# Kernel optimization log

Measured on AMD Instinct MI355X. Metric: run time of the kernel, lower is better.

Reference implementation:

```python
import jax, jax.numpy as jnp
import numpy as np

EPS = 1e-12  # matches torch F.normalize eps


def _l2_normalize(x, axis):
    n = jnp.linalg.norm(x, axis=axis, keepdims=True)
    return x / jnp.maximum(n, EPS)


def setup_inputs() -> dict:
    key = jax.random.key(0)
    k1, k2 = jax.random.split(key)
    B, C, h, w = 16, 64, 21, 21
    n_classes, M = 10, 2205  # M = shot(5) * h*w(441)
    x1 = jax.random.normal(k1, (B, C, h, w), dtype=jnp.float32)
    x2 = jax.random.normal(k2, (n_classes, C, M), dtype=jnp.float32)
    return {"x1": x1, "x2": x2, "neighbor_k": 3}


def reference(x1, x2, neighbor_k):
    B, C, h, w = x1.shape
    # queries: [B, h*w, C] local descriptors, L2-normalized per descriptor
    q = _l2_normalize(x1.reshape(B, C, h * w).transpose(0, 2, 1), axis=-1)
    # support: [n, C, M], normalized along channel dim (torch dim=0 per class)
    s = _l2_normalize(x2, axis=1)
    # all pairwise cosine similarities: [B, n, h*w, M]
    inner = jnp.einsum('bqc,ncm->bnqm', q, s)
    topv, _ = jax.lax.top_k(inner, neighbor_k)  # [B, n, h*w, k]
    return topv.sum(axis=(2, 3))  # [B, n]
```

## Files before the change

kernel.cpp:

```cpp
#include <hip/hip_runtime.h>
#include <math.h>

#define BB    16
#define CC    64
#define HW    441
#define QP    448
#define NCLS  10
#define MM    2205
#define MP2   2304
#define CH_T  8
#define CH_B  (CH_T * 16 * CC * 2)
#define NCH   18
#define NQT   4
#define NQG   7

typedef _Float16 half8 __attribute__((ext_vector_type(8)));
typedef float   float4_ __attribute__((ext_vector_type(4)));

#define WAIT_VMCNT(n) __builtin_amdgcn_s_waitcnt(0x0F70 | (n))

#define GLDS16(g, l) __builtin_amdgcn_global_load_lds(                         \
    (const __attribute__((address_space(1))) unsigned int*)(const void*)(g),   \
    (__attribute__((address_space(3))) unsigned int*)(void*)(l), 16, 0, 0)

__device__ __forceinline__ void ins3(float d, float& a0, float& a1, float& a2) {
    float n0 = fmaxf(d, a0);
    float n1 = __builtin_amdgcn_fmed3f(d, a0, a1);
    float n2 = __builtin_amdgcn_fmed3f(d, a1, a2);
    a0 = n0; a1 = n1; a2 = n2;
}

__global__ __launch_bounds__(256) void prep(const float* __restrict__ x1,
                                            const float* __restrict__ x2,
                                            _Float16* __restrict__ qn,
                                            _Float16* __restrict__ sn) {
    __shared__ float ssred[256];
    __shared__ half8 obuf[256];
    int tid = threadIdx.x;
    int ml = tid & 31, cg = tid >> 5;
    float v[8];
    half8* dstblk;
    int wz;
    if (blockIdx.x < BB * 14) {
        int b = blockIdx.x / 14, pt = blockIdx.x % 14;
        int p = pt * 32 + ml;
        const float* src = x1 + (size_t)b * CC * HW + p;
        bool real = p < HW;
        #pragma unroll
        for (int i = 0; i < 8; ++i) v[i] = real ? src[(size_t)(cg * 8 + i) * HW] : 0.f;
        wz = cg;
        dstblk = (half8*)(qn + ((size_t)(b * QP + pt * 32)) * CC);
    } else {
        int sb = blockIdx.x - BB * 14;
        int n = sb / 72, mt = sb % 72;
        int m = mt * 32 + ml;
        const float* src = x2 + (size_t)n * CC * MM + m;
        bool real = m < MM;
        #pragma unroll
        for (int i = 0; i < 8; ++i) v[i] = real ? src[(size_t)(cg * 8 + i) * MM] : 0.f;
        wz = cg ^ (ml & 7);
        dstblk = (half8*)(sn + ((size_t)(n * MP2 + mt * 32)) * CC);
    }
    float ss = 0.f;
    #pragma unroll
    for (int i = 0; i < 8; ++i) ss += v[i] * v[i];
    ssred[tid] = ss;
    __syncthreads();
    float tot = 0.f;
    #pragma unroll
    for (int j = 0; j < 8; ++j) tot += ssred[j * 32 + ml];
    float inv = 1.f / fmaxf(sqrtf(tot), 1e-12f);
    half8 h;
    #pragma unroll
    for (int i = 0; i < 8; ++i) h[i] = (_Float16)(v[i] * inv);
    obuf[ml * 8 + wz] = h;
    __syncthreads();
    dstblk[tid] = obuf[tid];
}

__global__ __launch_bounds__(256, 4) void img2class_mfma(const _Float16* __restrict__ qn,
                                                         const _Float16* __restrict__ sn,
                                                         float* __restrict__ out) {
    __shared__ half8 ldsv[2 * CH_T * 16 * 8];
    _Float16* ldsh = (_Float16*)ldsv;
    char* lbase = (char*)ldsv;

    int t  = blockIdx.x;
    int bn = t / NQG, qg = t % NQG;
    int b = bn / NCLS, n = bn % NCLS;

    int tid  = threadIdx.x;
    int wave = tid >> 6, lane = tid & 63;
    int col  = lane & 15, quad = lane >> 4;
    int q0 = qg * (NQT * 16);

    const char* sbase = (const char*)(sn + (size_t)n * MP2 * CC);
    int so   = wave * 4096 + lane * 16;
    int ldst = wave * 4096;

    #pragma unroll
    for (int i = 0; i < 4; ++i)
        GLDS16(sbase + so + i * 1024, lbase + ldst + i * 1024);

    const half8* Qp = (const half8*)(qn + ((size_t)(b * QP + q0 + col)) * CC) + quad;
    half8 Q0[NQT], Q1[NQT];
    #pragma unroll
    for (int qt = 0; qt < NQT; ++qt) {
        Q0[qt] = Qp[qt * 128];
        Q1[qt] = Qp[qt * 128 + 4];
    }

    float T0[NQT], T1[NQT], T2[NQT];
    #pragma unroll
    for (int qt = 0; qt < NQT; ++qt) { T0[qt] = -1.0e30f; T1[qt] = -1.0e30f; T2[qt] = -1.0e30f; }

    int offE0 = col * CC + ((quad       ^ (col & 7)) << 3);
    int offE1 = col * CC + (((4 + quad) ^ (col & 7)) << 3);

    for (int c = 0; c < NCH; ++c) {
        if (c + 1 < NCH) {
            __builtin_amdgcn_sched_barrier(0);
            const char* g = sbase + (size_t)(c + 1) * CH_B + so;
            char* l = lbase + ((c + 1) & 1) * CH_B + ldst;
            #pragma unroll
            for (int i = 0; i < 4; ++i)
                GLDS16(g + i * 1024, l + i * 1024);
            WAIT_VMCNT(4);
        } else {
            WAIT_VMCNT(0);
        }
        __builtin_amdgcn_sched_barrier(0);

        const _Float16* lw = ldsh + (c & 1) * (CH_T * 16 * CC) + wave * (32 * CC);
        half8 S0e = *(const half8*)(lw + offE0);
        half8 S1e = *(const half8*)(lw + offE1);
        half8 S0o = *(const half8*)(lw + offE0 + 16 * CC);
        half8 S1o = *(const half8*)(lw + offE1 + 16 * CC);

        int tE = c * CH_T + wave * 2;
        bool dopen = (tE >= 136);
        float pE0 = 0.f, pE1 = 0.f, pE2 = 0.f, pE3 = 0.f;
        float pO0 = 0.f, pO1 = 0.f, pO2 = 0.f, pO3 = 0.f;
        if (dopen) {
            int mE = tE * 16 + quad * 4;
            pE0 = (mE +  0 >= MM) ? -1.0e30f : 0.f;
            pE1 = (mE +  1 >= MM) ? -1.0e30f : 0.f;
            pE2 = (mE +  2 >= MM) ? -1.0e30f : 0.f;
            pE3 = (mE +  3 >= MM) ? -1.0e30f : 0.f;
            pO0 = (mE + 16 >= MM) ? -1.0e30f : 0.f;
            pO1 = (mE + 17 >= MM) ? -1.0e30f : 0.f;
            pO2 = (mE + 18 >= MM) ? -1.0e30f : 0.f;
            pO3 = (mE + 19 >= MM) ? -1.0e30f : 0.f;
        }

        float4_ z = {0.f, 0.f, 0.f, 0.f};
        #pragma unroll
        for (int qt = 0; qt < NQT; ++qt) {
            float4_ ae = __builtin_amdgcn_mfma_f32_16x16x32_f16(S0e, Q0[qt], z, 0, 0, 0);
            ae = __builtin_amdgcn_mfma_f32_16x16x32_f16(S1e, Q1[qt], ae, 0, 0, 0);
            float4_ ao = __builtin_amdgcn_mfma_f32_16x16x32_f16(S0o, Q0[qt], z, 0, 0, 0);
            ao = __builtin_amdgcn_mfma_f32_16x16x32_f16(S1o, Q1[qt], ao, 0, 0, 0);
            if (dopen) {
                ae.x += pE0; ae.y += pE1; ae.z += pE2; ae.w += pE3;
                ao.x += pO0; ao.y += pO1; ao.z += pO2; ao.w += pO3;
            }
            float d0 = fmaxf(ae.x, ao.x);
            float d1 = fmaxf(ae.y, ao.y);
            float d2 = fmaxf(ae.z, ao.z);
            float d3 = fmaxf(ae.w, ao.w);
            ins3(d0, T0[qt], T1[qt], T2[qt]);
            ins3(d1, T0[qt], T1[qt], T2[qt]);
            ins3(d2, T0[qt], T1[qt], T2[qt]);
            ins3(d3, T0[qt], T1[qt], T2[qt]);
        }
    }

    #pragma unroll
    for (int step = 16; step <= 32; step <<= 1) {
        #pragma unroll
        for (int qt = 0; qt < NQT; ++qt) {
            float o0 = __shfl_xor(T0[qt], step);
            float o1 = __shfl_xor(T1[qt], step);
            float o2 = __shfl_xor(T2[qt], step);
            ins3(o0, T0[qt], T1[qt], T2[qt]);
            ins3(o1, T0[qt], T1[qt], T2[qt]);
            ins3(o2, T0[qt], T1[qt], T2[qt]);
        }
    }

    float* dumpW = (float*)(lbase + wave * 4096);
    if (quad == 0) {
        #pragma unroll
        for (int qt = 0; qt < NQT; ++qt) {
            float* dp = dumpW + (qt * 16 + col) * 3;
            dp[0] = T0[qt]; dp[1] = T1[qt]; dp[2] = T2[qt];
        }
    }
    __syncthreads();

    float s = 0.f;
    if (tid < NQT * 16) {
        const float* d0 = (const float*)(lbase) + tid * 3;
        float a0 = d0[0], a1 = d0[1], a2 = d0[2];
        #pragma unroll
        for (int w = 1; w < 4; ++w) {
            const float* dw = (const float*)(lbase + w * 4096) + tid * 3;
            ins3(dw[0], a0, a1, a2);
            ins3(dw[1], a0, a1, a2);
            ins3(dw[2], a0, a1, a2);
        }
        s = a0 + a1 + a2;
    }
    #pragma unroll
    for (int step = 1; step < 64; step <<= 1) s += __shfl_xor(s, step);
    float* wsum = (float*)(lbase + CH_B);
    if (lane == 0) wsum[wave] = s;
    __syncthreads();
    if (tid == 0) atomicAdd(&out[bn], wsum[0] + wsum[1] + wsum[2] + wsum[3]);
}

extern "C" void kernel_launch(void* const* d_in, const int* in_sizes, int n_in,
                              void* d_out, int out_size, void* d_ws, size_t ws_size,
                              hipStream_t stream) {
    const float* x1 = (const float*)d_in[0];
    const float* x2 = (const float*)d_in[1];
    float* out = (float*)d_out;

    _Float16* qn = (_Float16*)d_ws;
    _Float16* sn = qn + (size_t)BB * QP * CC;

    hipMemsetAsync(d_out, 0, out_size, stream);
    prep<<<BB * 14 + NCLS * 72, 256, 0, stream>>>(x1, x2, qn, sn);
    img2class_mfma<<<BB * NCLS * NQG, 256, 0, stream>>>(qn, sn, out);
}
```

Before: 105.8 us.

## Share support chunks across all waves and split support dimension in halves

Every wave now processes all 128 support columns of each staged LDS chunk against its own 32 queries, so each block covers 128 queries instead of 64 and each chunk is reused across waves. The support dimension is split into two halves handled by separate blocks, with padding masked only on the final chunk. Per-query top-3 partials are written to workspace and combined by a new merge kernel, which replaces the atomics and the memset. The cost is extra block barriers per chunk, an extra kernel launch, and wasted work on padded queries (512 slots versus 441).

```diff
diff --git a/kernel.cpp b/kernel.cpp
--- a/kernel.cpp
+++ b/kernel.cpp
@@ -4,15 +4,14 @@
 #define BB    16
 #define CC    64
 #define HW    441
-#define QP    448
+#define QP2   512
 #define NCLS  10
 #define MM    2205
 #define MP2   2304
 #define CH_T  8
 #define CH_B  (CH_T * 16 * CC * 2)
-#define NCH   18
-#define NQT   4
-#define NQG   7
+#define NCH   9
+#define NQG   4
 
 typedef _Float16 half8 __attribute__((ext_vector_type(8)));
 typedef float   float4_ __attribute__((ext_vector_type(4)));
@@ -41,17 +40,17 @@
     float v[8];
     half8* dstblk;
     int wz;
-    if (blockIdx.x < BB * 14) {
-        int b = blockIdx.x / 14, pt = blockIdx.x % 14;
+    if (blockIdx.x < BB * 16) {
+        int b = blockIdx.x / 16, pt = blockIdx.x % 16;
         int p = pt * 32 + ml;
         const float* src = x1 + (size_t)b * CC * HW + p;
         bool real = p < HW;
         #pragma unroll
         for (int i = 0; i < 8; ++i) v[i] = real ? src[(size_t)(cg * 8 + i) * HW] : 0.f;
         wz = cg;
-        dstblk = (half8*)(qn + ((size_t)(b * QP + pt * 32)) * CC);
+        dstblk = (half8*)(qn + ((size_t)(b * QP2 + pt * 32)) * CC);
     } else {
-        int sb = blockIdx.x - BB * 14;
+        int sb = blockIdx.x - BB * 16;
         int n = sb / 72, mt = sb % 72;
         int m = mt * 32 + ml;
         const float* src = x2 + (size_t)n * CC * MM + m;
@@ -80,21 +79,23 @@
 
 __global__ __launch_bounds__(256, 4) void img2class_mfma(const _Float16* __restrict__ qn,
                                                          const _Float16* __restrict__ sn,
-                                                         float* __restrict__ out) {
+                                                         float* __restrict__ partial) {
     __shared__ half8 ldsv[2 * CH_T * 16 * 8];
     _Float16* ldsh = (_Float16*)ldsv;
     char* lbase = (char*)ldsv;
 
-    int t  = blockIdx.x;
+    int mh = blockIdx.x & 1;
+    int t  = blockIdx.x >> 1;
     int bn = t / NQG, qg = t % NQG;
     int b = bn / NCLS, n = bn % NCLS;
+    int mtile0 = mh ? 72 : 0;
 
     int tid  = threadIdx.x;
     int wave = tid >> 6, lane = tid & 63;
     int col  = lane & 15, quad = lane >> 4;
-    int q0 = qg * (NQT * 16);
-
-    const char* sbase = (const char*)(sn + (size_t)n * MP2 * CC);
+    int q0 = qg * 128;
+
+    const char* sbase = (const char*)(sn + (size_t)n * MP2 * CC) + (size_t)mtile0 * 16 * CC * 2;
     int so   = wave * 4096 + lane * 16;
     int ldst = wave * 4096;
 
@@ -102,24 +103,28 @@
     for (int i = 0; i < 4; ++i)
         GLDS16(sbase + so + i * 1024, lbase + ldst + i * 1024);
 
-    const half8* Qp = (const half8*)(qn + ((size_t)(b * QP + q0 + col)) * CC) + quad;
-    half8 Q0[NQT], Q1[NQT];
-    #pragma unroll
-    for (int qt = 0; qt < NQT; ++qt) {
-        Q0[qt] = Qp[qt * 128];
-        Q1[qt] = Qp[qt * 128 + 4];
-    }
-
-    float T0[NQT], T1[NQT], T2[NQT];
-    #pragma unroll
-    for (int qt = 0; qt < NQT; ++qt) { T0[qt] = -1.0e30f; T1[qt] = -1.0e30f; T2[qt] = -1.0e30f; }
-
-    int offE0 = col * CC + ((quad       ^ (col & 7)) << 3);
-    int offE1 = col * CC + (((4 + quad) ^ (col & 7)) << 3);
+    const half8* Qp = (const half8*)(qn + ((size_t)(b * QP2 + q0 + wave * 32 + col)) * CC) + quad;
+    half8 Q0[2], Q1[2];
+    #pragma unroll
+    for (int u = 0; u < 2; ++u) {
+        Q0[u] = Qp[u * 128];
+        Q1[u] = Qp[u * 128 + 4];
+    }
+
+    float T0[2], T1[2], T2[2];
+    #pragma unroll
+    for (int u = 0; u < 2; ++u) { T0[u] = -1.0e30f; T1[u] = -1.0e30f; T2[u] = -1.0e30f; }
+
+    int swz0 = (quad       ^ (col & 7)) << 3;
+    int swz1 = ((4 + quad) ^ (col & 7)) << 3;
+
+    float pO0 = (quad * 4 + 0 >= 13) ? -1.0e30f : 0.f;
+    float pO1 = (quad * 4 + 1 >= 13) ? -1.0e30f : 0.f;
+    float pO2 = (quad * 4 + 2 >= 13) ? -1.0e30f : 0.f;
+    float pO3 = (quad * 4 + 3 >= 13) ? -1.0e30f : 0.f;
 
     for (int c = 0; c < NCH; ++c) {
         if (c + 1 < NCH) {
-            __builtin_amdgcn_sched_barrier(0);
             const char* g = sbase + (size_t)(c + 1) * CH_B + so;
             char* l = lbase + ((c + 1) & 1) * CH_B + ldst;
             #pragma unroll
@@ -129,94 +134,84 @@
         } else {
             WAIT_VMCNT(0);
         }
+        __builtin_amdgcn_s_barrier();
         __builtin_amdgcn_sched_barrier(0);
 
-        const _Float16* lw = ldsh + (c & 1) * (CH_T * 16 * CC) + wave * (32 * CC);
-        half8 S0e = *(const half8*)(lw + offE0);
-        half8 S1e = *(const half8*)(lw + offE1);
-        half8 S0o = *(const half8*)(lw + offE0 + 16 * CC);
-        half8 S1o = *(const half8*)(lw + offE1 + 16 * CC);
-
-        int tE = c * CH_T + wave * 2;
-        bool dopen = (tE >= 136);
-        float pE0 = 0.f, pE1 = 0.f, pE2 = 0.f, pE3 = 0.f;
-        float pO0 = 0.f, pO1 = 0.f, pO2 = 0.f, pO3 = 0.f;
-        if (dopen) {
-            int mE = tE * 16 + quad * 4;
-            pE0 = (mE +  0 >= MM) ? -1.0e30f : 0.f;
-            pE1 = (mE +  1 >= MM) ? -1.0e30f : 0.f;
-            pE2 = (mE +  2 >= MM) ? -1.0e30f : 0.f;
-            pE3 = (mE +  3 >= MM) ? -1.0e30f : 0.f;
-            pO0 = (mE + 16 >= MM) ? -1.0e30f : 0.f;
-            pO1 = (mE + 17 >= MM) ? -1.0e30f : 0.f;
-            pO2 = (mE + 18 >= MM) ? -1.0e30f : 0.f;
-            pO3 = (mE + 19 >= MM) ? -1.0e30f : 0.f;
-        }
-
-        float4_ z = {0.f, 0.f, 0.f, 0.f};
-        #pragma unroll
-        for (int qt = 0; qt < NQT; ++qt) {
-            float4_ ae = __builtin_amdgcn_mfma_f32_16x16x32_f16(S0e, Q0[qt], z, 0, 0, 0);
-            ae = __builtin_amdgcn_mfma_f32_16x16x32_f16(S1e, Q1[qt], ae, 0, 0, 0);
-            float4_ ao = __builtin_amdgcn_mfma_f32_16x16x32_f16(S0o, Q0[qt], z, 0, 0, 0);
-            ao = __builtin_amdgcn_mfma_f32_16x16x32_f16(S1o, Q1[qt], ao, 0, 0, 0);
-            if (dopen) {
-                ae.x += pE0; ae.y += pE1; ae.z += pE2; ae.w += pE3;
-                ao.x += pO0; ao.y += pO1; ao.z += pO2; ao.w += pO3;
+        const _Float16* lw = ldsh + (c & 1) * (CH_T * 16 * CC);
+        bool lastc = (mh == 1) && (c == NCH - 1);
+        #pragma unroll
+        for (int p = 0; p < 4; ++p) {
+            if (lastc && p >= 1) break;
+            const _Float16* le = lw + (size_t)(p * 32 + col) * CC;
+            const _Float16* lo = le + 16 * CC;
+            half8 SA0 = *(const half8*)(le + swz0);
+            half8 SA1 = *(const half8*)(le + swz1);
+            half8 SB0 = *(const half8*)(lo + swz0);
+            half8 SB1 = *(const half8*)(lo + swz1);
+            float4_ z = {0.f, 0.f, 0.f, 0.f};
+            #pragma unroll
+            for (int u = 0; u < 2; ++u) {
+                float4_ ae = __builtin_amdgcn_mfma_f32_16x16x32_f16(SA0, Q0[u], z, 0, 0, 0);
+                ae = __builtin_amdgcn_mfma_f32_16x16x32_f16(SA1, Q1[u], ae, 0, 0, 0);
+                float4_ ao = __builtin_amdgcn_mfma_f32_16x16x32_f16(SB0, Q0[u], z, 0, 0, 0);
+                ao = __builtin_amdgcn_mfma_f32_16x16x32_f16(SB1, Q1[u], ao, 0, 0, 0);
+                if (lastc) { ao.x += pO0; ao.y += pO1; ao.z += pO2; ao.w += pO3; }
+                float d0 = fmaxf(ae.x, ao.x);
+                float d1 = fmaxf(ae.y, ao.y);
+                float d2 = fmaxf(ae.z, ao.z);
+                float d3 = fmaxf(ae.w, ao.w);
+                ins3(d0, T0[u], T1[u], T2[u]);
+                ins3(d1, T0[u], T1[u], T2[u]);
+                ins3(d2, T0[u], T1[u], T2[u]);
+                ins3(d3, T0[u], T1[u], T2[u]);
             }
-            float d0 = fmaxf(ae.x, ao.x);
-            float d1 = fmaxf(ae.y, ao.y);
-            float d2 = fmaxf(ae.z, ao.z);
-            float d3 = fmaxf(ae.w, ao.w);
-            ins3(d0, T0[qt], T1[qt], T2[qt]);
-            ins3(d1, T0[qt], T1[qt], T2[qt]);
-            ins3(d2, T0[qt], T1[qt], T2[qt]);
-            ins3(d3, T0[qt], T1[qt], T2[qt]);
-        }
+        }
+        __builtin_amdgcn_s_barrier();
     }
 
     #pragma unroll
     for (int step = 16; step <= 32; step <<= 1) {
         #pragma unroll
-        for (int qt = 0; qt < NQT; ++qt) {
-            float o0 = __shfl_xor(T0[qt], step);
-            float o1 = __shfl_xor(T1[qt], step);
-            float o2 = __shfl_xor(T2[qt], step);
-            ins3(o0, T0[qt], T1[qt], T2[qt]);
-            ins3(o1, T0[qt], T1[qt], T2[qt]);
-            ins3(o2, T0[qt], T1[qt], T2[qt]);
-        }
-    }
-
-    float* dumpW = (float*)(lbase + wave * 4096);
+        for (int u = 0; u < 2; ++u) {
+            float o0 = __shfl_xor(T0[u], step);
+            float o1 = __shfl_xor(T1[u], step);
+            float o2 = __shfl_xor(T2[u], step);
+            ins3(o0, T0[u], T1[u], T2[u]);
+            ins3(o1, T0[u], T1[u], T2[u]);
+            ins3(o2, T0[u], T1[u], T2[u]);
+        }
+    }
+
     if (quad == 0) {
         #pragma unroll
-        for (int qt = 0; qt < NQT; ++qt) {
-            float* dp = dumpW + (qt * 16 + col) * 3;
-            dp[0] = T0[qt]; dp[1] = T1[qt]; dp[2] = T2[qt];
-        }
-    }
+        for (int u = 0; u < 2; ++u) {
+            float* pp = partial + ((size_t)((bn * NQG + qg) * 2 + mh) * 128
+                                   + (wave * 2 + u) * 16 + col) * 3;
+            pp[0] = T0[u]; pp[1] = T1[u]; pp[2] = T2[u];
+        }
+    }
+}
+
+__global__ __launch_bounds__(512) void merge_halves(const float* __restrict__ partial,
+                                                    float* __restrict__ out) {
+    __shared__ float red[512];
+    int bn = blockIdx.x;
+    int q  = threadIdx.x;
+    int qg = q >> 7, ql = q & 127;
+    const float* p0 = partial + ((size_t)((bn * NQG + qg) * 2 + 0) * 128 + ql) * 3;
+    const float* p1 = partial + ((size_t)((bn * NQG + qg) * 2 + 1) * 128 + ql) * 3;
+    float a0 = p0[0], a1 = p0[1], a2 = p0[2];
+    ins3(p1[0], a0, a1, a2);
+    ins3(p1[1], a0, a1, a2);
+    ins3(p1[2], a0, a1, a2);
+    red[q] = a0 + a1 + a2;
     __syncthreads();
-
-    float s = 0.f;
-    if (tid < NQT * 16) {
-        const float* d0 = (const float*)(lbase) + tid * 3;
-        float a0 = d0[0], a1 = d0[1], a2 = d0[2];
-        #pragma unroll
-        for (int w = 1; w < 4; ++w) {
-            const float* dw = (const float*)(lbase + w * 4096) + tid * 3;
-            ins3(dw[0], a0, a1, a2);
-            ins3(dw[1], a0, a1, a2);
-            ins3(dw[2], a0, a1, a2);
-        }
-        s = a0 + a1 + a2;
-    }
-    #pragma unroll
-    for (int step = 1; step < 64; step <<= 1) s += __shfl_xor(s, step);
-    float* wsum = (float*)(lbase + CH_B);
-    if (lane == 0) wsum[wave] = s;
-    __syncthreads();
-    if (tid == 0) atomicAdd(&out[bn], wsum[0] + wsum[1] + wsum[2] + wsum[3]);
+    #pragma unroll
+    for (int stride = 256; stride >= 1; stride >>= 1) {
+        if (q < stride) red[q] += red[q + stride];
+        __syncthreads();
+    }
+    if (q == 0) out[bn] = red[0];
 }
 
 extern "C" void kernel_launch(void* const* d_in, const int* in_sizes, int n_in,
@@ -226,10 +221,11 @@
     const float* x2 = (const float*)d_in[1];
     float* out = (float*)d_out;
 
-    _Float16* qn = (_Float16*)d_ws;
-    _Float16* sn = qn + (size_t)BB * QP * CC;
-
-    hipMemsetAsync(d_out, 0, out_size, stream);
-    prep<<<BB * 14 + NCLS * 72, 256, 0, stream>>>(x1, x2, qn, sn);
-    img2class_mfma<<<BB * NCLS * NQG, 256, 0, stream>>>(qn, sn, out);
-}
+    _Float16* qn   = (_Float16*)d_ws;
+    _Float16* sn   = qn + (size_t)BB * QP2 * CC;
+    float* partial = (float*)(sn + (size_t)NCLS * MP2 * CC);
+
+    prep<<<BB * 16 + NCLS * 72, 256, 0, stream>>>(x1, x2, qn, sn);
+    img2class_mfma<<<BB * NCLS * NQG * 2, 256, 0, stream>>>(qn, sn, partial);
+    merge_halves<<<BB * NCLS, 512, 0, stream>>>(partial, out);
+}
```

Measured after the change: 98.34 us. 1.08x faster.

## Split support dimension across two blocks, triple-buffer LDS, merge halves in new kernel

Applied to the files above, without the earlier changes.

Each (batch, class, query-group) block is split into two blocks that each scan half of the support descriptors. This doubles the grid and halves the serial chunk loop per block. The LDS ring grows to three buffers with a prefetch distance of two chunks, and the chunk loop is fully unrolled. Per-query top-3 partials go to workspace, and a new merge kernel combines the halves and reduces per (b, n), replacing the memset and atomics. The cost is an extra kernel launch, more LDS per block, and a round trip of partials through global memory.

```diff
diff --git a/kernel.cpp b/kernel.cpp
--- a/kernel.cpp
+++ b/kernel.cpp
@@ -10,9 +10,8 @@
 #define MP2   2304
 #define CH_T  8
 #define CH_B  (CH_T * 16 * CC * 2)
-#define NCH   18
+#define NCH   9
 #define NQT   4
-#define NQG   7
 
 typedef _Float16 half8 __attribute__((ext_vector_type(8)));
 typedef float   float4_ __attribute__((ext_vector_type(4)));
@@ -80,27 +79,32 @@
 
 __global__ __launch_bounds__(256, 4) void img2class_mfma(const _Float16* __restrict__ qn,
                                                          const _Float16* __restrict__ sn,
-                                                         float* __restrict__ out) {
-    __shared__ half8 ldsv[2 * CH_T * 16 * 8];
+                                                         float* __restrict__ partial) {
+    __shared__ half8 ldsv[3 * CH_T * 16 * 8];
     _Float16* ldsh = (_Float16*)ldsv;
     char* lbase = (char*)ldsv;
 
-    int t  = blockIdx.x;
-    int bn = t / NQG, qg = t % NQG;
+    int mh = blockIdx.x & 1;
+    int t  = blockIdx.x >> 1;
+    int bn = t / 7, qg = t % 7;
     int b = bn / NCLS, n = bn % NCLS;
+    int mtile0 = mh ? 72 : 0;
 
     int tid  = threadIdx.x;
     int wave = tid >> 6, lane = tid & 63;
     int col  = lane & 15, quad = lane >> 4;
     int q0 = qg * (NQT * 16);
 
-    const char* sbase = (const char*)(sn + (size_t)n * MP2 * CC);
+    const char* sbase = (const char*)(sn + (size_t)n * MP2 * CC) + (size_t)mtile0 * 16 * CC * 2;
     int so   = wave * 4096 + lane * 16;
     int ldst = wave * 4096;
 
     #pragma unroll
     for (int i = 0; i < 4; ++i)
         GLDS16(sbase + so + i * 1024, lbase + ldst + i * 1024);
+    #pragma unroll
+    for (int i = 0; i < 4; ++i)
+        GLDS16(sbase + CH_B + so + i * 1024, lbase + CH_B + ldst + i * 1024);
 
     const half8* Qp = (const half8*)(qn + ((size_t)(b * QP + q0 + col)) * CC) + quad;
     half8 Q0[NQT], Q1[NQT];
@@ -117,40 +121,41 @@
     int offE0 = col * CC + ((quad       ^ (col & 7)) << 3);
     int offE1 = col * CC + (((4 + quad) ^ (col & 7)) << 3);
 
+    #pragma unroll
     for (int c = 0; c < NCH; ++c) {
-        if (c + 1 < NCH) {
-            __builtin_amdgcn_sched_barrier(0);
-            const char* g = sbase + (size_t)(c + 1) * CH_B + so;
-            char* l = lbase + ((c + 1) & 1) * CH_B + ldst;
+        __builtin_amdgcn_sched_barrier(0);
+        if (c + 2 < NCH) {
+            const char* g = sbase + (size_t)(c + 2) * CH_B + so;
+            char* l = lbase + ((c + 2) % 3) * CH_B + ldst;
             #pragma unroll
             for (int i = 0; i < 4; ++i)
                 GLDS16(g + i * 1024, l + i * 1024);
+            __builtin_amdgcn_sched_barrier(0);
+            WAIT_VMCNT(8);
+        } else if (c + 1 < NCH) {
             WAIT_VMCNT(4);
         } else {
             WAIT_VMCNT(0);
         }
         __builtin_amdgcn_sched_barrier(0);
 
-        const _Float16* lw = ldsh + (c & 1) * (CH_T * 16 * CC) + wave * (32 * CC);
+        bool lastc = (mh == 1) && (c == NCH - 1);
+        if (lastc && wave >= 1) continue;
+
+        const _Float16* lw = ldsh + (c % 3) * (CH_T * 16 * CC) + wave * (32 * CC);
         half8 S0e = *(const half8*)(lw + offE0);
         half8 S1e = *(const half8*)(lw + offE1);
         half8 S0o = *(const half8*)(lw + offE0 + 16 * CC);
         half8 S1o = *(const half8*)(lw + offE1 + 16 * CC);
 
-        int tE = c * CH_T + wave * 2;
-        bool dopen = (tE >= 136);
-        float pE0 = 0.f, pE1 = 0.f, pE2 = 0.f, pE3 = 0.f;
+        int tE = mtile0 + c * CH_T + wave * 2;
         float pO0 = 0.f, pO1 = 0.f, pO2 = 0.f, pO3 = 0.f;
-        if (dopen) {
-            int mE = tE * 16 + quad * 4;
-            pE0 = (mE +  0 >= MM) ? -1.0e30f : 0.f;
-            pE1 = (mE +  1 >= MM) ? -1.0e30f : 0.f;
-            pE2 = (mE +  2 >= MM) ? -1.0e30f : 0.f;
-            pE3 = (mE +  3 >= MM) ? -1.0e30f : 0.f;
-            pO0 = (mE + 16 >= MM) ? -1.0e30f : 0.f;
-            pO1 = (mE + 17 >= MM) ? -1.0e30f : 0.f;
-            pO2 = (mE + 18 >= MM) ? -1.0e30f : 0.f;
-            pO3 = (mE + 19 >= MM) ? -1.0e30f : 0.f;
+        if (lastc) {
+            int mO = tE * 16 + 16 + quad * 4;
+            pO0 = (mO + 0 >= MM) ? -1.0e30f : 0.f;
+            pO1 = (mO + 1 >= MM) ? -1.0e30f : 0.f;
+            pO2 = (mO + 2 >= MM) ? -1.0e30f : 0.f;
+            pO3 = (mO + 3 >= MM) ? -1.0e30f : 0.f;
         }
 
         float4_ z = {0.f, 0.f, 0.f, 0.f};
@@ -160,10 +165,7 @@
             ae = __builtin_amdgcn_mfma_f32_16x16x32_f16(S1e, Q1[qt], ae, 0, 0, 0);
             float4_ ao = __builtin_amdgcn_mfma_f32_16x16x32_f16(S0o, Q0[qt], z, 0, 0, 0);
             ao = __builtin_amdgcn_mfma_f32_16x16x32_f16(S1o, Q1[qt], ao, 0, 0, 0);
-            if (dopen) {
-                ae.x += pE0; ae.y += pE1; ae.z += pE2; ae.w += pE3;
-                ao.x += pO0; ao.y += pO1; ao.z += pO2; ao.w += pO3;
-            }
+            if (lastc) { ao.x += pO0; ao.y += pO1; ao.z += pO2; ao.w += pO3; }
             float d0 = fmaxf(ae.x, ao.x);
             float d1 = fmaxf(ae.y, ao.y);
             float d2 = fmaxf(ae.z, ao.z);
@@ -198,8 +200,7 @@
     }
     __syncthreads();
 
-    float s = 0.f;
-    if (tid < NQT * 16) {
+    if (tid < 64) {
         const float* d0 = (const float*)(lbase) + tid * 3;
         float a0 = d0[0], a1 = d0[1], a2 = d0[2];
         #pragma unroll
@@ -209,14 +210,35 @@
             ins3(dw[1], a0, a1, a2);
             ins3(dw[2], a0, a1, a2);
         }
+        float* pp = partial + ((size_t)((bn * 7 + qg) * 2 + mh) * 64 + tid) * 3;
+        pp[0] = a0; pp[1] = a1; pp[2] = a2;
+    }
+}
+
+__global__ __launch_bounds__(512) void merge_halves(const float* __restrict__ partial,
+                                                    float* __restrict__ out) {
+    __shared__ float red[512];
+    int bn = blockIdx.x;
+    int q  = threadIdx.x;
+    float s = 0.f;
+    if (q < HW) {
+        int qg = q >> 6, ql = q & 63;
+        const float* p0 = partial + ((size_t)((bn * 7 + qg) * 2 + 0) * 64 + ql) * 3;
+        const float* p1 = partial + ((size_t)((bn * 7 + qg) * 2 + 1) * 64 + ql) * 3;
+        float a0 = p0[0], a1 = p0[1], a2 = p0[2];
+        ins3(p1[0], a0, a1, a2);
+        ins3(p1[1], a0, a1, a2);
+        ins3(p1[2], a0, a1, a2);
         s = a0 + a1 + a2;
     }
-    #pragma unroll
-    for (int step = 1; step < 64; step <<= 1) s += __shfl_xor(s, step);
-    float* wsum = (float*)(lbase + CH_B);
-    if (lane == 0) wsum[wave] = s;
-    __syncthreads();
-    if (tid == 0) atomicAdd(&out[bn], wsum[0] + wsum[1] + wsum[2] + wsum[3]);
+    red[q] = s;
+    __syncthreads();
+    #pragma unroll
+    for (int stride = 256; stride >= 1; stride >>= 1) {
+        if (q < stride) red[q] += red[q + stride];
+        __syncthreads();
+    }
+    if (q == 0) out[bn] = red[0];
 }
 
 extern "C" void kernel_launch(void* const* d_in, const int* in_sizes, int n_in,
@@ -226,10 +248,11 @@
     const float* x2 = (const float*)d_in[1];
     float* out = (float*)d_out;
 
-    _Float16* qn = (_Float16*)d_ws;
-    _Float16* sn = qn + (size_t)BB * QP * CC;
-
-    hipMemsetAsync(d_out, 0, out_size, stream);
+    _Float16* qn   = (_Float16*)d_ws;
+    _Float16* sn   = qn + (size_t)BB * QP * CC;
+    float* partial = (float*)(sn + (size_t)NCLS * MP2 * CC);
+
     prep<<<BB * 14 + NCLS * 72, 256, 0, stream>>>(x1, x2, qn, sn);
-    img2class_mfma<<<BB * NCLS * NQG, 256, 0, stream>>>(qn, sn, out);
-}
+    img2class_mfma<<<BB * NCLS * 7 * 2, 256, 0, stream>>>(qn, sn, partial);
+    merge_halves<<<BB * NCLS, 512, 0, stream>>>(partial, out);
+}
```

Measured after the change: 99.00 us. -6.4%, faster.
